# Performance work log

Measured on AMD Instinct MI355X. Metric: run time of the kernel, lower is better.

The kernel has to match this reference:

```python
import jax, jax.numpy as jnp
import numpy as np

# hps: rnn_size=512, num_mixture=5, input_seq_width=35, output_seq_width=32,
#      batch_size=128, max_seq_len=1000
B, T, D_IN, Z, H, K = 128, 1000, 35, 32, 512, 5
OUT = 3 * K * Z  # 3 * num_mixture * output_seq_width = 480


def setup_inputs() -> dict:
    key = jax.random.key(0)
    ks = jax.random.split(key, 5)
    scale = 0.05
    return {
        "inputs": jax.random.normal(ks[0], (B, T, D_IN), jnp.float32),
        # Keras LSTMCell params: kernel [D,4H], recurrent_kernel [H,4H], bias [4H]
        # gate order: i, f, g(candidate), o
        "Wk": jax.random.normal(ks[1], (D_IN, 4 * H), jnp.float32) * scale,
        "Wr": jax.random.normal(ks[2], (H, 4 * H), jnp.float32) * scale,
        "b": jnp.zeros((4 * H,), jnp.float32),
        # MDN Dense head: [H, 3*K*Z]
        "Wd": jax.random.normal(ks[3], (H, OUT), jnp.float32) * scale,
        "bd": jnp.zeros((OUT,), jnp.float32),
    }


def reference(inputs, Wk, Wr, b, Wd, bd):
    # split into (vae_z, a) then concat back -> identity, kept for faithfulness
    vae_z, a = inputs[..., :Z], inputs[..., Z:]
    z_a = jnp.concatenate([vae_z, a], axis=2)  # [B, T, D_IN]

    # precompute input projection for all timesteps (hoisted out of the scan)
    xz = jnp.einsum('btd,dk->btk', z_a, Wk) + b  # [B, T, 4H]
    xz_t = jnp.swapaxes(xz, 0, 1)                # [T, B, 4H]

    h0 = jnp.zeros((z_a.shape[0], H), xz.dtype)

    def step(carry, xt):
        h, c = carry
        gates = xt + h @ Wr  # [B, 4H]
        i, f, g, o = jnp.split(gates, 4, axis=-1)
        c = jax.nn.sigmoid(f) * c + jax.nn.sigmoid(i) * jnp.tanh(g)
        h = jax.nn.sigmoid(o) * jnp.tanh(c)
        return (h, c), h

    _, hs = jax.lax.scan(step, (h0, h0), xz_t)   # hs: [T, B, H]
    rnn_out = jnp.swapaxes(hs, 0, 1).reshape(-1, H)  # [B*T, H]
    out = rnn_out @ Wd + bd  # [B*T, 3*K*Z] mu/logstd/logpi MDN params
    return out
```

## Files before the change

kernel.cpp:

```cpp
#include <hip/hip_runtime.h>


#define NGRP   8
#define NSLICE 32
#define GB     16
#define HH     512
#define TT     1000
#define DIN    35
#define OUTC   480
#define ODC    15
#define HWORDS 2048

typedef __bf16 bf16x8 __attribute__((ext_vector_type(8)));
typedef float  f32x4  __attribute__((ext_vector_type(4)));
typedef unsigned short u16;
typedef unsigned int   u32;
typedef unsigned long long u64;

__device__ __forceinline__ u16 f2bf(float x) {
    u32 u = __float_as_uint(x);
    u += 0x7FFFu + ((u >> 16) & 1u);
    return (u16)(u >> 16);
}
__device__ __forceinline__ u32 pk2(float a, float b) {
    return (u32)f2bf(a) | ((u32)f2bf(b) << 16);
}
__device__ __forceinline__ float sigf(float x) { return 1.0f / (1.0f + __expf(-x)); }
__device__ __forceinline__ float tanh_fast(float x) {
    float ax = fabsf(x);
    float e = __expf(-2.0f * ax);
    return copysignf((1.0f - e) / (1.0f + e), x);
}

union bf8u { u32 u[4]; bf16x8 v; };

#define BARRIER() do { asm volatile("" ::: "memory"); \
                       __builtin_amdgcn_s_barrier(); \
                       asm volatile("" ::: "memory"); \
                       __builtin_amdgcn_sched_barrier(0); } while (0)
#define WAIT_LGKM() do { asm volatile("s_waitcnt lgkmcnt(0)" ::: "memory"); \
                         __builtin_amdgcn_sched_barrier(0); } while (0)
#define WAIT_VM()   do { asm volatile("s_waitcnt vmcnt(0)" ::: "memory"); \
                         __builtin_amdgcn_sched_barrier(0); } while (0)

#define MFMA16(a, b, c) __builtin_amdgcn_mfma_f32_16x16x32_bf16((a), (b), (c), 0, 0, 0)

__global__ void __launch_bounds__(512, 1)
mdn_kernel(const float* __restrict__ inp, const float* __restrict__ Wk,
           const float* __restrict__ Wr,  const float* __restrict__ bg,
           const float* __restrict__ Wd,  const float* __restrict__ bd,
           float* __restrict__ out, u32* __restrict__ flags, u64* __restrict__ hbuf)
{
    __shared__ __attribute__((aligned(16))) u16  wr_s[64 * HH];
    __shared__ __attribute__((aligned(16))) u16  wk_s[64 * 64];
    __shared__ __attribute__((aligned(16))) u16  wd_s[16 * HH];
    __shared__ __attribute__((aligned(16))) u16  h_s [GB * HH];
    __shared__ __attribute__((aligned(16))) float gbuf[4 * 16 * 16];
    __shared__ __attribute__((aligned(16))) float pbuf[4 * 16 * 16];

    const int tid  = threadIdx.x;
    const int lane = tid & 63;
    const int wave = tid >> 6;
    const int g    = blockIdx.x & 7;
    const int s    = blockIdx.x >> 3;
    const int m16  = lane & 15;
    const int kq   = lane >> 4;

    {
        int n = tid & 63;
        int q = n >> 4, j4 = n & 15;
        int col = q * HH + s * 16 + j4;
        for (int k = tid >> 6; k < HH; k += 8)
            wr_s[n * HH + (k ^ ((n & 7) << 3))] = f2bf(Wr[(size_t)k * 2048 + col]);
        for (int k = tid >> 6; k < 64; k += 8)
            wk_s[n * 64 + (k ^ ((n & 7) << 3))] = f2bf(k < DIN ? Wk[(size_t)k * 2048 + col] : 0.0f);
    }
    {
        int n = tid & 15;
        for (int k = tid >> 4; k < HH; k += 32)
            wd_s[n * HH + (k ^ ((n & 7) << 3))] =
                f2bf(n < ODC ? Wd[(size_t)k * OUTC + s * ODC + n] : 0.0f);
    }
    for (int i = tid; i < GB * HH / 4; i += 512) ((u64*)h_s)[i] = 0ull;
    __syncthreads();

    bf16x8 bfr[18];
    if (wave < 4) {
        int n = wave * 16 + m16;
        #pragma unroll
        for (int ks = 0; ks < 16; ++ks) {
            int k0 = 32 * ks + 8 * kq;
            bfr[ks] = *(const bf16x8*)(&wr_s[n * HH + (k0 ^ ((n & 7) << 3))]);
        }
        #pragma unroll
        for (int i = 0; i < 2; ++i) {
            int k0 = 32 * i + 8 * kq;
            bfr[16 + i] = *(const bf16x8*)(&wk_s[n * 64 + (k0 ^ ((n & 7) << 3))]);
        }
    } else {
        int w4 = wave - 4;
        #pragma unroll
        for (int kk = 0; kk < 4; ++kk) {
            int k0 = w4 * 128 + 32 * kk + 8 * kq;
            bfr[kk] = *(const bf16x8*)(&wd_s[m16 * HH + (k0 ^ ((m16 & 7) << 3))]);
        }
    }

    float c_reg = 0.f;
    float bi = 0.f, bff = 0.f, bgg = 0.f, boo = 0.f, bdv = 0.f;
    int br = 0, jj = 0, oo = 0;
    if (tid < 256) {
        br = tid >> 4; jj = tid & 15;
        int scol = s * 16 + jj;
        bi  = bg[0 * HH + scol];
        bff = bg[1 * HH + scol];
        bgg = bg[2 * HH + scol];
        boo = bg[3 * HH + scol];
    } else {
        br = (tid - 256) >> 4; oo = (tid - 256) & 15;
        if (oo < ODC) bdv = bd[s * ODC + oo];
    }

    float xr[8];
    float xe0 = 0.f, xe1 = 0.f, xe2 = 0.f;
    #pragma unroll
    for (int i = 0; i < 8; ++i) xr[i] = 0.f;
    if (wave < 4) {
        const float* ip = inp + ((size_t)(g * GB + m16) * TT + 0) * DIN;
        #pragma unroll
        for (int i = 0; i < 8; ++i) xr[i] = ip[kq * 8 + i];
        if (kq == 0) { xe0 = ip[32]; xe1 = ip[33]; xe2 = ip[34]; }
    }
    __syncthreads();

    const int pb = tid >> 5;
    const int pk = tid & 31;

    for (int t = 0; t <= TT; ++t) {
        if (wave < 4) {
            if (t < TT) {
                bf8u a0, a1;
                a0.u[0] = pk2(xr[0], xr[1]); a0.u[1] = pk2(xr[2], xr[3]);
                a0.u[2] = pk2(xr[4], xr[5]); a0.u[3] = pk2(xr[6], xr[7]);
                a1.u[0] = (kq == 0) ? pk2(xe0, xe1) : 0u;
                a1.u[1] = (kq == 0) ? pk2(xe2, 0.f) : 0u;
                a1.u[2] = 0u; a1.u[3] = 0u;
                f32x4 acc0 = {0,0,0,0}, acc1 = {0,0,0,0};
                acc0 = MFMA16(a0.v, bfr[16], acc0);
                acc1 = MFMA16(a1.v, bfr[17], acc1);
                #pragma unroll
                for (int ks = 0; ks < 16; ks += 2) {
                    int k0 = 32 * ks + 8 * kq;
                    bf16x8 a = *(const bf16x8*)(&h_s[m16 * HH + (k0 ^ ((m16 & 7) << 3))]);
                    acc0 = MFMA16(a, bfr[ks], acc0);
                    int k1 = 32 * (ks + 1) + 8 * kq;
                    bf16x8 a2 = *(const bf16x8*)(&h_s[m16 * HH + (k1 ^ ((m16 & 7) << 3))]);
                    acc1 = MFMA16(a2, bfr[ks + 1], acc1);
                }
                #pragma unroll
                for (int j = 0; j < 4; ++j)
                    gbuf[wave * 256 + (kq * 4 + j) * 16 + m16] = acc0[j] + acc1[j];
            }
        } else {
            if (t > 0) {
                int w4 = wave - 4;
                f32x4 acc0 = {0,0,0,0}, acc1 = {0,0,0,0};
                #pragma unroll
                for (int kk = 0; kk < 4; kk += 2) {
                    int k0 = w4 * 128 + 32 * kk + 8 * kq;
                    bf16x8 a = *(const bf16x8*)(&h_s[m16 * HH + (k0 ^ ((m16 & 7) << 3))]);
                    acc0 = MFMA16(a, bfr[kk], acc0);
                    int k1 = w4 * 128 + 32 * (kk + 1) + 8 * kq;
                    bf16x8 a2 = *(const bf16x8*)(&h_s[m16 * HH + (k1 ^ ((m16 & 7) << 3))]);
                    acc1 = MFMA16(a2, bfr[kk + 1], acc1);
                }
                #pragma unroll
                for (int j = 0; j < 4; ++j)
                    pbuf[w4 * 256 + (kq * 4 + j) * 16 + m16] = acc0[j] + acc1[j];
            }
        }
        WAIT_LGKM(); BARRIER();

        if (tid < 256) {
            if (t < TT) {
                float iv = gbuf[0 * 256 + br * 16 + jj] + bi;
                float fv = gbuf[1 * 256 + br * 16 + jj] + bff;
                float gv = gbuf[2 * 256 + br * 16 + jj] + bgg;
                float ov = gbuf[3 * 256 + br * 16 + jj] + boo;
                c_reg = sigf(fv) * c_reg + sigf(iv) * tanh_fast(gv);
                float h = sigf(ov) * tanh_fast(c_reg);
                u32 hb32 = (u32)f2bf(h);
                u32 o1 = (u32)__shfl_xor((int)hb32, 1);
                u32 lo = hb32 | (o1 << 16);
                u32 o2 = (u32)__shfl_xor((int)lo, 2);
                if ((jj & 3) == 0) {
                    u64 w = (u64)lo | ((u64)o2 << 32);
                    u64* dst = hbuf + (size_t)(t & 1) * (NGRP * HWORDS) + g * HWORDS
                                  + br * 128 + s * 4 + (jj >> 2);
                    __hip_atomic_store(dst, w, __ATOMIC_RELAXED, __HIP_MEMORY_SCOPE_AGENT);
                }
            }
        } else {
            if (t > 0) {
                float v = pbuf[0 * 256 + br * 16 + oo] + pbuf[1 * 256 + br * 16 + oo]
                        + pbuf[2 * 256 + br * 16 + oo] + pbuf[3 * 256 + br * 16 + oo] + bdv;
                if (oo < ODC)
                    out[((size_t)(g * GB + br) * TT + (t - 1)) * OUTC + s * ODC + oo] = v;
            }
        }

        if (t < TT) {
            if (wave < 4) WAIT_VM();
            BARRIER();
            if (tid == 0)
                __hip_atomic_store(&flags[(g * NSLICE + s) * 16], (u32)(t + 1),
                                   __ATOMIC_RELAXED, __HIP_MEMORY_SCOPE_AGENT);
            if (wave < 4 && t + 1 < TT) {
                const float* ip = inp + ((size_t)(g * GB + m16) * TT + (t + 1)) * DIN;
                #pragma unroll
                for (int i = 0; i < 8; ++i) xr[i] = ip[kq * 8 + i];
                if (kq == 0) { xe0 = ip[32]; xe1 = ip[33]; xe2 = ip[34]; }
            }
            if (wave == 0) {
                const u32* fp = flags + (g * NSLICE + (lane & 31)) * 16;
                const u32 tgt = (u32)(t + 1);
                int spins = 0;
                while (true) {
                    u32 v = __hip_atomic_load(fp, __ATOMIC_RELAXED, __HIP_MEMORY_SCOPE_AGENT);
                    if (__all((int)(v >= tgt))) break;
                    __builtin_amdgcn_s_sleep(1);
                    if (++spins > (1 << 20)) break;
                }
            }
            BARRIER();
            {
                const u64* bp = hbuf + (size_t)(t & 1) * (NGRP * HWORDS) + g * HWORDS;
                #pragma unroll
                for (int i = 0; i < 2; ++i) {
                    int widx = pb * 128 + pk * 2 + i * 64;
                    u64 vlo = __hip_atomic_load(bp + widx,     __ATOMIC_RELAXED, __HIP_MEMORY_SCOPE_AGENT);
                    u64 vhi = __hip_atomic_load(bp + widx + 1, __ATOMIC_RELAXED, __HIP_MEMORY_SCOPE_AGENT);
                    int k  = pk * 8 + i * 256;
                    int sk = k ^ ((pb & 7) << 3);
                    *(u64*)(&h_s[pb * HH + sk])     = vlo;
                    *(u64*)(&h_s[pb * HH + sk + 4]) = vhi;
                }
            }
            WAIT_LGKM(); BARRIER();
        }
    }
}

extern "C" void kernel_launch(void* const* d_in, const int* in_sizes, int n_in,
                              void* d_out, int out_size, void* d_ws, size_t ws_size,
                              hipStream_t stream) {
    const float* inp = (const float*)d_in[0];
    const float* Wk  = (const float*)d_in[1];
    const float* Wr  = (const float*)d_in[2];
    const float* bg  = (const float*)d_in[3];
    const float* Wd  = (const float*)d_in[4];
    const float* bd  = (const float*)d_in[5];
    float* out = (float*)d_out;

    char* ws = (char*)d_ws;
    u32* flags = (u32*)ws;
    u64* hbuf  = (u64*)(ws + 16384);
    hipMemsetAsync(d_ws, 0, 16384, stream);

    hipLaunchKernelGGL(mdn_kernel, dim3(NGRP * NSLICE), dim3(512), 0, stream,
                       inp, Wk, Wr, bg, Wd, bd, out, flags, hbuf);
}
```

Baseline: 2.819 ms.

## Fuse gate activations into MFMA waves and publish per-wave flags

```diff
diff --git a/kernel.cpp b/kernel.cpp
--- a/kernel.cpp
+++ b/kernel.cpp
@@ -22,14 +22,14 @@
     u += 0x7FFFu + ((u >> 16) & 1u);
     return (u16)(u >> 16);
 }
-__device__ __forceinline__ u32 pk2(float a, float b) {
-    return (u32)f2bf(a) | ((u32)f2bf(b) << 16);
-}
 __device__ __forceinline__ float sigf(float x) { return 1.0f / (1.0f + __expf(-x)); }
 __device__ __forceinline__ float tanh_fast(float x) {
     float ax = fabsf(x);
     float e = __expf(-2.0f * ax);
     return copysignf((1.0f - e) / (1.0f + e), x);
+}
+__device__ __forceinline__ u32 pk2f(float a, float b) {
+    return (u32)f2bf(a) | ((u32)f2bf(b) << 16);
 }
 
 union bf8u { u32 u[4]; bf16x8 v; };
@@ -55,8 +55,8 @@
     __shared__ __attribute__((aligned(16))) u16  wk_s[64 * 64];
     __shared__ __attribute__((aligned(16))) u16  wd_s[16 * HH];
     __shared__ __attribute__((aligned(16))) u16  h_s [GB * HH];
-    __shared__ __attribute__((aligned(16))) float gbuf[4 * 16 * 16];
-    __shared__ __attribute__((aligned(16))) float pbuf[4 * 16 * 16];
+    __shared__ __attribute__((aligned(16))) float gbuf[4 * 256];
+    __shared__ __attribute__((aligned(16))) float pbuf[2 * 4 * 256];
 
     const int tid  = threadIdx.x;
     const int lane = tid & 63;
@@ -86,16 +86,16 @@
 
     bf16x8 bfr[18];
     if (wave < 4) {
-        int n = wave * 16 + m16;
+        int nloc = (m16 & 3) * 16 + 4 * wave + (m16 >> 2);
         #pragma unroll
         for (int ks = 0; ks < 16; ++ks) {
             int k0 = 32 * ks + 8 * kq;
-            bfr[ks] = *(const bf16x8*)(&wr_s[n * HH + (k0 ^ ((n & 7) << 3))]);
+            bfr[ks] = *(const bf16x8*)(&wr_s[nloc * HH + (k0 ^ ((nloc & 7) << 3))]);
         }
         #pragma unroll
         for (int i = 0; i < 2; ++i) {
             int k0 = 32 * i + 8 * kq;
-            bfr[16 + i] = *(const bf16x8*)(&wk_s[n * 64 + (k0 ^ ((n & 7) << 3))]);
+            bfr[16 + i] = *(const bf16x8*)(&wk_s[nloc * 64 + (k0 ^ ((nloc & 7) << 3))]);
         }
     } else {
         int w4 = wave - 4;
@@ -108,16 +108,17 @@
 
     float c_reg = 0.f;
     float bi = 0.f, bff = 0.f, bgg = 0.f, boo = 0.f, bdv = 0.f;
-    int br = 0, jj = 0, oo = 0;
-    if (tid < 256) {
-        br = tid >> 4; jj = tid & 15;
+    const int cb = lane & 15;
+    const int ce = lane >> 4;
+    if (wave < 4) {
+        int jj = 4 * wave + ce;
         int scol = s * 16 + jj;
         bi  = bg[0 * HH + scol];
         bff = bg[1 * HH + scol];
         bgg = bg[2 * HH + scol];
         boo = bg[3 * HH + scol];
     } else {
-        br = (tid - 256) >> 4; oo = (tid - 256) & 15;
+        int oo = lane & 15;
         if (oo < ODC) bdv = bd[s * ODC + oo];
     }
 
@@ -136,14 +137,14 @@
     const int pb = tid >> 5;
     const int pk = tid & 31;
 
-    for (int t = 0; t <= TT; ++t) {
+    for (int t = 0; t <= TT + 1; ++t) {
         if (wave < 4) {
             if (t < TT) {
                 bf8u a0, a1;
-                a0.u[0] = pk2(xr[0], xr[1]); a0.u[1] = pk2(xr[2], xr[3]);
-                a0.u[2] = pk2(xr[4], xr[5]); a0.u[3] = pk2(xr[6], xr[7]);
-                a1.u[0] = (kq == 0) ? pk2(xe0, xe1) : 0u;
-                a1.u[1] = (kq == 0) ? pk2(xe2, 0.f) : 0u;
+                a0.u[0] = pk2f(xr[0], xr[1]); a0.u[1] = pk2f(xr[2], xr[3]);
+                a0.u[2] = pk2f(xr[4], xr[5]); a0.u[3] = pk2f(xr[6], xr[7]);
+                a1.u[0] = (kq == 0) ? pk2f(xe0, xe1) : 0u;
+                a1.u[1] = (kq == 0) ? pk2f(xe2, 0.f) : 0u;
                 a1.u[2] = 0u; a1.u[3] = 0u;
                 f32x4 acc0 = {0,0,0,0}, acc1 = {0,0,0,0};
                 acc0 = MFMA16(a0.v, bfr[16], acc0);
@@ -160,10 +161,36 @@
                 #pragma unroll
                 for (int j = 0; j < 4; ++j)
                     gbuf[wave * 256 + (kq * 4 + j) * 16 + m16] = acc0[j] + acc1[j];
+                WAIT_LGKM();
+                f32x4 gv = *(const f32x4*)(&gbuf[wave * 256 + cb * 16 + 4 * ce]);
+                float iv = gv[0] + bi, fv = gv[1] + bff;
+                float gg2 = gv[2] + bgg, ov = gv[3] + boo;
+                c_reg = sigf(fv) * c_reg + sigf(iv) * tanh_fast(gg2);
+                float h = sigf(ov) * tanh_fast(c_reg);
+                u32 hb32 = (u32)f2bf(h);
+                u32 o1 = (u32)__shfl_xor((int)hb32, 16);
+                u32 pair = ((ce & 1) == 0) ? (hb32 | (o1 << 16)) : (o1 | (hb32 << 16));
+                u32 o2 = (u32)__shfl_xor((int)pair, 32);
+                if (ce == 0) {
+                    u64 w64 = (u64)pair | ((u64)o2 << 32);
+                    u64* dst = hbuf + (size_t)(t & 1) * (NGRP * HWORDS) + g * HWORDS
+                                  + cb * 128 + s * 4 + wave;
+                    __hip_atomic_store(dst, w64, __ATOMIC_RELAXED, __HIP_MEMORY_SCOPE_AGENT);
+                }
+                WAIT_VM();
+                if (lane == 0)
+                    __hip_atomic_store(&flags[(g * 128 + s * 4 + wave) * 16], (u32)(t + 1),
+                                       __ATOMIC_RELAXED, __HIP_MEMORY_SCOPE_AGENT);
+                if (t + 1 < TT) {
+                    const float* ip = inp + ((size_t)(g * GB + m16) * TT + (t + 1)) * DIN;
+                    #pragma unroll
+                    for (int i = 0; i < 8; ++i) xr[i] = ip[kq * 8 + i];
+                    if (kq == 0) { xe0 = ip[32]; xe1 = ip[33]; xe2 = ip[34]; }
+                }
             }
         } else {
-            if (t > 0) {
-                int w4 = wave - 4;
+            int w4 = wave - 4;
+            if (t >= 1 && t <= TT) {
                 f32x4 acc0 = {0,0,0,0}, acc1 = {0,0,0,0};
                 #pragma unroll
                 for (int kk = 0; kk < 4; kk += 2) {
@@ -176,60 +203,33 @@
                 }
                 #pragma unroll
                 for (int j = 0; j < 4; ++j)
-                    pbuf[w4 * 256 + (kq * 4 + j) * 16 + m16] = acc0[j] + acc1[j];
-            }
-        }
-        WAIT_LGKM(); BARRIER();
-
-        if (tid < 256) {
-            if (t < TT) {
-                float iv = gbuf[0 * 256 + br * 16 + jj] + bi;
-                float fv = gbuf[1 * 256 + br * 16 + jj] + bff;
-                float gv = gbuf[2 * 256 + br * 16 + jj] + bgg;
-                float ov = gbuf[3 * 256 + br * 16 + jj] + boo;
-                c_reg = sigf(fv) * c_reg + sigf(iv) * tanh_fast(gv);
-                float h = sigf(ov) * tanh_fast(c_reg);
-                u32 hb32 = (u32)f2bf(h);
-                u32 o1 = (u32)__shfl_xor((int)hb32, 1);
-                u32 lo = hb32 | (o1 << 16);
-                u32 o2 = (u32)__shfl_xor((int)lo, 2);
-                if ((jj & 3) == 0) {
-                    u64 w = (u64)lo | ((u64)o2 << 32);
-                    u64* dst = hbuf + (size_t)(t & 1) * (NGRP * HWORDS) + g * HWORDS
-                                  + br * 128 + s * 4 + (jj >> 2);
-                    __hip_atomic_store(dst, w, __ATOMIC_RELAXED, __HIP_MEMORY_SCOPE_AGENT);
-                }
-            }
-        } else {
-            if (t > 0) {
-                float v = pbuf[0 * 256 + br * 16 + oo] + pbuf[1 * 256 + br * 16 + oo]
-                        + pbuf[2 * 256 + br * 16 + oo] + pbuf[3 * 256 + br * 16 + oo] + bdv;
+                    pbuf[(t & 1) * 1024 + w4 * 256 + (kq * 4 + j) * 16 + m16] = acc0[j] + acc1[j];
+            }
+            if (t >= 2) {
+                int bb = 4 * w4 + (lane >> 4);
+                int oo = lane & 15;
+                int par = ((t & 1) ^ 1) * 1024;
+                float v = pbuf[par + 0 * 256 + bb * 16 + oo]
+                        + pbuf[par + 1 * 256 + bb * 16 + oo]
+                        + pbuf[par + 2 * 256 + bb * 16 + oo]
+                        + pbuf[par + 3 * 256 + bb * 16 + oo] + bdv;
                 if (oo < ODC)
-                    out[((size_t)(g * GB + br) * TT + (t - 1)) * OUTC + s * ODC + oo] = v;
+                    out[((size_t)(g * GB + bb) * TT + (t - 2)) * OUTC + s * ODC + oo] = v;
             }
         }
 
         if (t < TT) {
-            if (wave < 4) WAIT_VM();
-            BARRIER();
-            if (tid == 0)
-                __hip_atomic_store(&flags[(g * NSLICE + s) * 16], (u32)(t + 1),
-                                   __ATOMIC_RELAXED, __HIP_MEMORY_SCOPE_AGENT);
-            if (wave < 4 && t + 1 < TT) {
-                const float* ip = inp + ((size_t)(g * GB + m16) * TT + (t + 1)) * DIN;
-                #pragma unroll
-                for (int i = 0; i < 8; ++i) xr[i] = ip[kq * 8 + i];
-                if (kq == 0) { xe0 = ip[32]; xe1 = ip[33]; xe2 = ip[34]; }
-            }
             if (wave == 0) {
-                const u32* fp = flags + (g * NSLICE + (lane & 31)) * 16;
+                const u32* f0 = flags + (g * 128 + lane) * 16;
+                const u32* f1 = flags + (g * 128 + 64 + lane) * 16;
                 const u32 tgt = (u32)(t + 1);
                 int spins = 0;
                 while (true) {
-                    u32 v = __hip_atomic_load(fp, __ATOMIC_RELAXED, __HIP_MEMORY_SCOPE_AGENT);
-                    if (__all((int)(v >= tgt))) break;
+                    u32 a = __hip_atomic_load(f0, __ATOMIC_RELAXED, __HIP_MEMORY_SCOPE_AGENT);
+                    u32 b = __hip_atomic_load(f1, __ATOMIC_RELAXED, __HIP_MEMORY_SCOPE_AGENT);
+                    if (__all((int)(a >= tgt && b >= tgt))) break;
                     __builtin_amdgcn_s_sleep(1);
-                    if (++spins > (1 << 20)) break;
+                    if (++spins > (1 << 18)) break;
                 }
             }
             BARRIER();
@@ -246,6 +246,8 @@
                     *(u64*)(&h_s[pb * HH + sk + 4]) = vhi;
                 }
             }
+            WAIT_LGKM(); BARRIER();
+        } else {
             WAIT_LGKM(); BARRIER();
         }
     }
@@ -264,8 +266,8 @@
 
     char* ws = (char*)d_ws;
     u32* flags = (u32*)ws;
-    u64* hbuf  = (u64*)(ws + 16384);
-    hipMemsetAsync(d_ws, 0, 16384, stream);
+    u64* hbuf  = (u64*)(ws + 65536);
+    hipMemsetAsync(d_ws, 0, 65536, stream);
 
     hipLaunchKernelGGL(mdn_kernel, dim3(NGRP * NSLICE), dim3(512), 0, stream,
                        inp, Wk, Wr, bg, Wd, bd, out, flags, hbuf);
```

After: 2.993 ms. 6.2% more time.
